# Kernel tuning notes

Measured on AMD Instinct MI355X. Metric: run time of the kernel, lower is better.

## Reference

```python
import jax, jax.numpy as jnp
import numpy as np

B, N, D = 4, 2048, 1024
DF = 4 * D
EPS = 1e-5


def _layernorm(x, w, b):
    mu = jnp.mean(x, axis=-1, keepdims=True)
    var = jnp.mean(jnp.square(x - mu), axis=-1, keepdims=True)
    return (x - mu) * jax.lax.rsqrt(var + EPS) * w + b


def setup_inputs() -> dict:
    key = jax.random.key(0)
    ks = jax.random.split(key, 8)
    x = jax.random.normal(ks[0], (B, N, D), dtype=jnp.float32)
    # conv filter param (torch init is zeros; use small randn for numeric coverage)
    weights = jax.random.normal(ks[1], (1, 1, N), dtype=jnp.float32) * 0.02
    # registered buffer: sqrt(1/(i+1)) per token, shape (1, N, 1)
    scale = jnp.sqrt(1.0 / (jnp.arange(N, dtype=jnp.float32) + 1.0))[None, :, None]
    ln1_w = jnp.ones((D,), jnp.float32)
    ln1_b = jnp.zeros((D,), jnp.float32)
    W1 = jax.random.normal(ks[2], (DF, D), dtype=jnp.float32) * 0.02
    b1 = jnp.zeros((DF,), jnp.float32)
    W2 = jax.random.normal(ks[3], (D, DF), dtype=jnp.float32) * 0.02
    b2 = jnp.zeros((D,), jnp.float32)
    scalar = jax.random.normal(ks[4], (1,), dtype=jnp.float32) * 0.1
    ln2_w = jnp.ones((D,), jnp.float32)
    ln2_b = jnp.zeros((D,), jnp.float32)
    return dict(x=x, weights=weights, scale=scale, ln1_w=ln1_w, ln1_b=ln1_b,
                W1=W1, b1=b1, W2=W2, b2=b2, scalar=scalar, ln2_w=ln2_w, ln2_b=ln2_b)


def reference(x, weights, scale, ln1_w, ln1_b, W1, b1, W2, b2, scalar, ln2_w, ln2_b):
    n = weights.shape[-1]
    # FFT token-mixing conv: operate over token axis. x: (B,N,D) -> (B,D,N)
    xt = jnp.swapaxes(x, -2, -1)
    # real inputs -> rfft/irfft equals real(ifft(fft*fft)) from the torch code
    prod = jnp.fft.rfft(xt, n=2 * n) * jnp.fft.rfft(weights, n=2 * n)
    conv = jnp.fft.irfft(prod, n=2 * n)[..., :n]  # (B,D,N)
    x1 = jnp.swapaxes(conv, -2, -1)               # (B,N,D)
    x1 = _layernorm(x + x1 * scale, ln1_w, ln1_b)
    # GELU MLP (torch F.gelu default = exact erf gelu)
    h = jax.nn.gelu(jnp.einsum('bnd,fd->bnf', x1, W1) + b1, approximate=False)
    mlp = jnp.einsum('bnf,df->bnd', h, W2) + b2
    x2 = _layernorm(x1 + scalar * mlp, ln2_w, ln2_b)
    return x2
```

## Files before the change

### kernel.cpp

```cpp
#include <hip/hip_runtime.h>
#include <cstdint>

typedef float floatx4 __attribute__((ext_vector_type(4)));
typedef int intx8 __attribute__((ext_vector_type(8)));

__device__ __forceinline__ unsigned short f2b(float f) {
  union { float f; unsigned u; } v; v.f = f;
  return (unsigned short)((v.u + 0x7FFFu + ((v.u >> 16) & 1u)) >> 16);
}
__device__ __forceinline__ float b2f(unsigned short h) {
  union { unsigned u; float f; } v; v.u = ((unsigned)h) << 16;
  return v.f;
}

__device__ __forceinline__ void gload_lds16(const void* g, void* l) {
  __builtin_amdgcn_global_load_lds(
      (const __attribute__((address_space(1))) void*)g,
      (__attribute__((address_space(3))) void*)l, 16, 0, 0);
}


__global__ void cast_f8x64_kernel(const float* __restrict__ in,
                                  int* __restrict__ out) {
  long i = (long)blockIdx.x * 256 + threadIdx.x;
  float4 v = ((const float4*)in)[i];
  int pk = __builtin_amdgcn_cvt_pk_fp8_f32(v.x * 64.0f, v.y * 64.0f, 0, false);
  pk = __builtin_amdgcn_cvt_pk_fp8_f32(v.z * 64.0f, v.w * 64.0f, pk, true);
  out[i] = pk;
}

__global__ void build_T8_kernel(const float* __restrict__ w,
                                int* __restrict__ T8) {
  long i = (long)blockIdx.x * 256 + threadIdx.x;
  int n = (int)(i >> 9);
  int m0 = (int)(i & 511) * 4;
  float v[4];
#pragma unroll
  for (int r = 0; r < 4; ++r) {
    int m = m0 + r;
    v[r] = (m <= n) ? w[n - m] * 64.0f : 0.0f;
  }
  int pk = __builtin_amdgcn_cvt_pk_fp8_f32(v[0], v[1], 0, false);
  pk = __builtin_amdgcn_cvt_pk_fp8_f32(v[2], v[3], pk, true);
  T8[i] = pk;
}

__global__ void transpose_cast_f8_kernel(const float* __restrict__ x,
                                         unsigned char* __restrict__ xT) {
  __shared__ float tile[32][33];
  int b = blockIdx.z;
  int n0 = blockIdx.y * 32;
  int d0 = blockIdx.x * 32;
  int tx = threadIdx.x;
  int ty = threadIdx.y;
  for (int i = ty; i < 32; i += 8)
    tile[i][tx] = x[((long)b * 2048 + n0 + i) * 1024 + d0 + tx];
  __syncthreads();
  float a = tile[ty * 4 + 0][tx];
  float c = tile[ty * 4 + 1][tx];
  float e = tile[ty * 4 + 2][tx];
  float f = tile[ty * 4 + 3][tx];
  int pk = __builtin_amdgcn_cvt_pk_fp8_f32(a, c, 0, false);
  pk = __builtin_amdgcn_cvt_pk_fp8_f32(e, f, pk, true);
  *(int*)(xT + ((long)b * 1024 + d0 + tx) * 2048 + n0 + ty * 4) = pk;
}

template <int EPI, int NT, bool TRI>
__global__ __launch_bounds__(256, 2) void gemm_f8(
    const unsigned char* __restrict__ A, const unsigned char* __restrict__ B,
    int Kstride, int Kloop, long zsA, long zsB, long zsC,
    int rx, int ryb, int gxn, unsigned sclA, unsigned sclB,
    const float* __restrict__ resid, const float* __restrict__ scale,
    const float* __restrict__ bias,
    float* __restrict__ Cf, unsigned short* __restrict__ Cb,
    unsigned char* __restrict__ C8) {
  __shared__ __align__(16) unsigned char As[2 * 16 * 1040];
  __shared__ __align__(16) unsigned char Bs[2 * 16 * 1040];
  const int tid = threadIdx.x;
  const int wid = tid >> 6;
  const int lane = tid & 63;
  const int quad = lane >> 4;
  const int l16 = lane & 15;
  const int wm = (wid >> 1) * 64;
  const int wn = (wid & 1) * 64;

  const int bid = blockIdx.x;
  const int xcd = bid & 7;
  const int ib = bid >> 3;
  const int ci = ib % rx;
  const int ri = ib / rx;
  long bm, bn;
  if (TRI) {
    bm = (long)(ri == 0 ? xcd : 15 - xcd) * 128;
    bn = (long)ci * 128;
  } else {
    const int gx = xcd % gxn;
    const int gy = xcd / gxn;
    bm = (long)(gy * ryb + ri) * 128;
    bn = (long)(gx * rx + ci) * 128;
  }
  const int bz = blockIdx.z;
  const unsigned char* Ab = A + zsA * bz;
  const unsigned char* Bb = B + zsB * bz;

  floatx4 acc[4][4];
#pragma unroll
  for (int i = 0; i < 4; ++i)
#pragma unroll
    for (int j = 0; j < 4; ++j)
      acc[i][j] = floatx4{0.0f, 0.0f, 0.0f, 0.0f};

  const int srow = tid >> 3;
  const int scol = (tid & 7) * 16;
  const unsigned char* gA[4];
  const unsigned char* gB[4];
  unsigned char* lA[4];
  unsigned char* lB[4];
#pragma unroll
  for (int p = 0; p < 4; ++p) {
    gA[p] = Ab + (bm + p * 32 + srow) * (long)Kstride + scol;
    gB[p] = Bb + (bn + p * 32 + srow) * (long)Kstride + scol;
    lA[p] = As + (p * 4 + wid) * 1040;
    lB[p] = Bs + (p * 4 + wid) * 1040;
  }

  int offA[4], offB[4];
#pragma unroll
  for (int i = 0; i < 4; ++i) {
    const int ra = wm + i * 16 + l16;
    offA[i] = (ra >> 3) * 1040 + (ra & 7) * 128 + quad * 32;
    const int rb = wn + i * 16 + l16;
    offB[i] = (rb >> 3) * 1040 + (rb & 7) * 128 + quad * 32;
  }

  const int kend = TRI ? min(Kloop, (int)bm + 128) : Kloop;

#pragma unroll
  for (int p = 0; p < 4; ++p) {
    gload_lds16(gA[p], lA[p]);
    gload_lds16(gB[p], lB[p]);
  }

  int so = 0;
  for (int kk = 0; kk < kend; kk += 128) {
    const int kn = kk + 128;
    if (kn < kend) {
      const int po = so ^ 16640;
#pragma unroll
      for (int p = 0; p < 4; ++p) {
        gload_lds16(gA[p] + kn, lA[p] + po);
        gload_lds16(gB[p] + kn, lB[p] + po);
      }
      asm volatile("s_waitcnt vmcnt(8)" ::: "memory");
    } else {
      asm volatile("s_waitcnt vmcnt(0)" ::: "memory");
    }
    __builtin_amdgcn_s_barrier();

    intx8 af[4], bfr[4];
#pragma unroll
    for (int i = 0; i < 4; ++i) {
      union { intx8 v; int4 q[2]; } u;
      u.q[0] = *(const int4*)(As + so + offA[i]);
      u.q[1] = *(const int4*)(As + so + offA[i] + 16);
      af[i] = u.v;
    }
#pragma unroll
    for (int j = 0; j < 4; ++j) {
      union { intx8 v; int4 q[2]; } u;
      u.q[0] = *(const int4*)(Bs + so + offB[j]);
      u.q[1] = *(const int4*)(Bs + so + offB[j] + 16);
      bfr[j] = u.v;
    }
    __builtin_amdgcn_s_setprio(1);
#pragma unroll
    for (int i = 0; i < 4; ++i)
#pragma unroll
      for (int j = 0; j < 4; ++j)
        acc[i][j] = __builtin_amdgcn_mfma_scale_f32_16x16x128_f8f6f4(
            af[i], bfr[j], acc[i][j], 0 , 0 ,
            0, sclA, 0, sclB);
    __builtin_amdgcn_s_setprio(0);
    __builtin_amdgcn_s_barrier();
    so ^= 16640;
  }

#pragma unroll
  for (int i = 0; i < 4; ++i)
#pragma unroll
    for (int j = 0; j < 4; ++j)
#pragma unroll
      for (int r = 0; r < 4; ++r) {
        long row = bm + wm + i * 16 + quad * 4 + r;
        long col = bn + wn + j * 16 + l16;
        long idx = (long)bz * zsC + row * (long)NT + col;
        float v = acc[i][j][r];
        if (EPI == 0) {
          Cb[idx] = f2b(v);
        } else if (EPI == 1) {
          Cf[idx] = resid[idx] + scale[row] * v;
        } else {
          v += bias[col];
          float u = v * (0.7978845608f + 0.0356774081f * v * v);
          float u2 = u * u;
          float t = __fdividef(u * (15.0f + u2), 15.0f + 6.0f * u2);
          t = fminf(fmaxf(t, -1.0f), 1.0f);
          float g = 0.5f * v * (1.0f + t);
          int pk = __builtin_amdgcn_cvt_pk_fp8_f32(g, 0.0f, 0, false);
          C8[idx] = (unsigned char)(pk & 0xFF);
        }
      }
}

__global__ __launch_bounds__(256) void ln_kernel(
    const float* __restrict__ in, const float* __restrict__ w,
    const float* __restrict__ b, unsigned short* __restrict__ outb,
    int* __restrict__ outf8) {
  const long row = blockIdx.x;
  const int tid = threadIdx.x;
  float4 v = ((const float4*)in)[row * 256 + tid];
  float s = v.x + v.y + v.z + v.w;
  float ss = v.x * v.x + v.y * v.y + v.z * v.z + v.w * v.w;
#pragma unroll
  for (int off = 32; off > 0; off >>= 1) {
    s += __shfl_down(s, off);
    ss += __shfl_down(ss, off);
  }
  __shared__ float red[8];
  const int wid = tid >> 6, lane = tid & 63;
  if (lane == 0) { red[wid] = s; red[4 + wid] = ss; }
  __syncthreads();
  s = red[0] + red[1] + red[2] + red[3];
  ss = red[4] + red[5] + red[6] + red[7];
  const float mu = s * (1.0f / 1024.0f);
  const float var = ss * (1.0f / 1024.0f) - mu * mu;
  const float rs = rsqrtf(var + 1e-5f);
  float4 wv = ((const float4*)w)[tid];
  float4 bv = ((const float4*)b)[tid];
  float o0 = (v.x - mu) * rs * wv.x + bv.x;
  float o1 = (v.y - mu) * rs * wv.y + bv.y;
  float o2 = (v.z - mu) * rs * wv.z + bv.z;
  float o3 = (v.w - mu) * rs * wv.w + bv.w;
  ushort4 u{f2b(o0), f2b(o1), f2b(o2), f2b(o3)};
  ((ushort4*)outb)[row * 256 + tid] = u;
  int pk = __builtin_amdgcn_cvt_pk_fp8_f32(o0, o1, 0, false);
  pk = __builtin_amdgcn_cvt_pk_fp8_f32(o2, o3, pk, true);
  outf8[row * 256 + tid] = pk;
}

__global__ __launch_bounds__(256) void ln2_fused_kernel(
    const unsigned short* __restrict__ y0, const unsigned short* __restrict__ y1,
    const unsigned short* __restrict__ x1b, const float* __restrict__ b2,
    const float* __restrict__ scalar_p, const float* __restrict__ w,
    const float* __restrict__ b, float* __restrict__ out) {
  const long row = blockIdx.x;
  const int tid = threadIdx.x;
  ushort4 a4 = ((const ushort4*)y0)[row * 256 + tid];
  ushort4 c4 = ((const ushort4*)y1)[row * 256 + tid];
  ushort4 xr = ((const ushort4*)x1b)[row * 256 + tid];
  float4 bias = ((const float4*)b2)[tid];
  const float scl = scalar_p[0];
  float4 v;
  v.x = b2f(xr.x) + scl * (b2f(a4.x) + b2f(c4.x) + bias.x);
  v.y = b2f(xr.y) + scl * (b2f(a4.y) + b2f(c4.y) + bias.y);
  v.z = b2f(xr.z) + scl * (b2f(a4.z) + b2f(c4.z) + bias.z);
  v.w = b2f(xr.w) + scl * (b2f(a4.w) + b2f(c4.w) + bias.w);
  float s = v.x + v.y + v.z + v.w;
  float ss = v.x * v.x + v.y * v.y + v.z * v.z + v.w * v.w;
#pragma unroll
  for (int off = 32; off > 0; off >>= 1) {
    s += __shfl_down(s, off);
    ss += __shfl_down(ss, off);
  }
  __shared__ float red[8];
  const int wid = tid >> 6, lane = tid & 63;
  if (lane == 0) { red[wid] = s; red[4 + wid] = ss; }
  __syncthreads();
  s = red[0] + red[1] + red[2] + red[3];
  ss = red[4] + red[5] + red[6] + red[7];
  const float mu = s * (1.0f / 1024.0f);
  const float var = ss * (1.0f / 1024.0f) - mu * mu;
  const float rs = rsqrtf(var + 1e-5f);
  float4 wv = ((const float4*)w)[tid];
  float4 bv = ((const float4*)b)[tid];
  float4 o;
  o.x = (v.x - mu) * rs * wv.x + bv.x;
  o.y = (v.y - mu) * rs * wv.y + bv.y;
  o.z = (v.z - mu) * rs * wv.z + bv.z;
  o.w = (v.w - mu) * rs * wv.w + bv.w;
  ((float4*)out)[row * 256 + tid] = o;
}

extern "C" void kernel_launch(void* const* d_in, const int* in_sizes, int n_in,
                              void* d_out, int out_size, void* d_ws, size_t ws_size,
                              hipStream_t stream) {
  const float* x      = (const float*)d_in[0];
  const float* wconv  = (const float*)d_in[1];
  const float* scale  = (const float*)d_in[2];
  const float* ln1w   = (const float*)d_in[3];
  const float* ln1b   = (const float*)d_in[4];
  const float* W1     = (const float*)d_in[5];
  const float* b1     = (const float*)d_in[6];
  const float* W2     = (const float*)d_in[7];
  const float* b2     = (const float*)d_in[8];
  const float* scalar = (const float*)d_in[9];
  const float* ln2w   = (const float*)d_in[10];
  const float* ln2b   = (const float*)d_in[11];
  float* out = (float*)d_out;

  const unsigned SCL_1  = 0x7F7F7F7Fu;
  const unsigned SCL_64 = 0x79797979u;

  char* ws = (char*)d_ws;
  unsigned char* xT8   = (unsigned char*)ws;  ws += (size_t)4 * 1024 * 2048;
  unsigned char* T8    = (unsigned char*)ws;  ws += (size_t)2048 * 2048;
  unsigned char* W1f8  = (unsigned char*)ws;  ws += (size_t)4096 * 1024;
  unsigned char* W2f8  = (unsigned char*)ws;  ws += (size_t)4096 * 1024;
  float* y             = (float*)ws;          ws += (size_t)8192 * 1024 * 4;
  unsigned short* yb   = (unsigned short*)ws; ws += (size_t)2 * 8192 * 1024 * 2;
  unsigned short* x1b  = (unsigned short*)ws; ws += (size_t)8192 * 1024 * 2;
  unsigned char* x1f8  = (unsigned char*)ws;  ws += (size_t)8192 * 1024;
  unsigned char* h8    = (unsigned char*)ws;  ws += (size_t)8192 * 4096;

  cast_f8x64_kernel<<<4096, 256, 0, stream>>>(W1, (int*)W1f8);
  cast_f8x64_kernel<<<4096, 256, 0, stream>>>(W2, (int*)W2f8);
  build_T8_kernel<<<4096, 256, 0, stream>>>(wconv, (int*)T8);
  transpose_cast_f8_kernel<<<dim3(32, 64, 4), dim3(32, 8), 0, stream>>>(x, xT8);

  gemm_f8<1, 1024, true><<<dim3(128, 1, 4), 256, 0, stream>>>(
      T8, xT8, 2048, 2048, 0L, (long)1024 * 2048, (long)2048 * 1024,
      8, 0, 0, SCL_64, SCL_1, x, scale, nullptr, y, nullptr, nullptr);
  ln_kernel<<<8192, 256, 0, stream>>>(y, ln1w, ln1b, x1b, (int*)x1f8);
  gemm_f8<2, 4096, false><<<dim3(2048, 1, 1), 256, 0, stream>>>(
      x1f8, W1f8, 1024, 1024, 0L, 0L, 0L,
      16, 16, 2, SCL_1, SCL_64, nullptr, nullptr, b1, nullptr, nullptr, h8);
  gemm_f8<0, 1024, false><<<dim3(512, 1, 2), 256, 0, stream>>>(
      h8, W2f8, 4096, 2048, 2048L, 2048L, (long)8192 * 1024,
      8, 8, 1, SCL_1, SCL_64, nullptr, nullptr, nullptr, nullptr, yb, nullptr);
  ln2_fused_kernel<<<8192, 256, 0, stream>>>(
      yb, yb + (size_t)8192 * 1024, x1b, b2, scalar, ln2w, ln2b, out);
}
```

Baseline: 297.9 us.

## Use 256x256-tile 512-thread FP8 GEMM for MLP; single-buffer conv GEMM

Adds a new gemm_f8_256 kernel with 256x256 output tiles, 8 waves and double-buffered LDS, and uses it for both MLP GEMMs. Larger tiles raise data reuse per LDS load and cut global traffic. The original 128x128 kernel, still used for the triangular conv GEMM, drops its double buffering and priority hints so it can run at 4 blocks per CU, trading load/compute overlap for occupancy. Fewer, larger blocks may hurt wave balance across CUs, and the extra accumulators raise register pressure.

After: 301.1 us. Within noise of the previous version (+1.1%).

```diff
diff --git a/kernel.cpp b/kernel.cpp
--- a/kernel.cpp
+++ b/kernel.cpp
@@ -66,7 +66,7 @@
 }
 
 template <int EPI, int NT, bool TRI>
-__global__ __launch_bounds__(256, 2) void gemm_f8(
+__global__ __launch_bounds__(256, 4) void gemm_f8(
     const unsigned char* __restrict__ A, const unsigned char* __restrict__ B,
     int Kstride, int Kloop, long zsA, long zsB, long zsC,
     int rx, int ryb, int gxn, unsigned sclA, unsigned sclB,
@@ -74,8 +74,8 @@
     const float* __restrict__ bias,
     float* __restrict__ Cf, unsigned short* __restrict__ Cb,
     unsigned char* __restrict__ C8) {
-  __shared__ __align__(16) unsigned char As[2 * 16 * 1040];
-  __shared__ __align__(16) unsigned char Bs[2 * 16 * 1040];
+  __shared__ __align__(16) unsigned char As[16 * 1040];
+  __shared__ __align__(16) unsigned char Bs[16 * 1040];
   const int tid = threadIdx.x;
   const int wid = tid >> 6;
   const int lane = tid & 63;
@@ -124,55 +124,34 @@
     lB[p] = Bs + (p * 4 + wid) * 1040;
   }
 
-  int offA[4], offB[4];
-#pragma unroll
-  for (int i = 0; i < 4; ++i) {
-    const int ra = wm + i * 16 + l16;
-    offA[i] = (ra >> 3) * 1040 + (ra & 7) * 128 + quad * 32;
-    const int rb = wn + i * 16 + l16;
-    offB[i] = (rb >> 3) * 1040 + (rb & 7) * 128 + quad * 32;
-  }
-
   const int kend = TRI ? min(Kloop, (int)bm + 128) : Kloop;
-
-#pragma unroll
-  for (int p = 0; p < 4; ++p) {
-    gload_lds16(gA[p], lA[p]);
-    gload_lds16(gB[p], lB[p]);
-  }
-
-  int so = 0;
   for (int kk = 0; kk < kend; kk += 128) {
-    const int kn = kk + 128;
-    if (kn < kend) {
-      const int po = so ^ 16640;
-#pragma unroll
-      for (int p = 0; p < 4; ++p) {
-        gload_lds16(gA[p] + kn, lA[p] + po);
-        gload_lds16(gB[p] + kn, lB[p] + po);
-      }
-      asm volatile("s_waitcnt vmcnt(8)" ::: "memory");
-    } else {
-      asm volatile("s_waitcnt vmcnt(0)" ::: "memory");
-    }
-    __builtin_amdgcn_s_barrier();
-
+    __syncthreads();
+#pragma unroll
+    for (int p = 0; p < 4; ++p) {
+      gload_lds16(gA[p] + kk, lA[p]);
+      gload_lds16(gB[p] + kk, lB[p]);
+    }
+    __syncthreads();
     intx8 af[4], bfr[4];
 #pragma unroll
     for (int i = 0; i < 4; ++i) {
+      const int ra = wm + i * 16 + l16;
+      const int off = (ra >> 3) * 1040 + (ra & 7) * 128 + quad * 32;
       union { intx8 v; int4 q[2]; } u;
-      u.q[0] = *(const int4*)(As + so + offA[i]);
-      u.q[1] = *(const int4*)(As + so + offA[i] + 16);
+      u.q[0] = *(const int4*)(As + off);
+      u.q[1] = *(const int4*)(As + off + 16);
       af[i] = u.v;
     }
 #pragma unroll
     for (int j = 0; j < 4; ++j) {
+      const int rb = wn + j * 16 + l16;
+      const int off = (rb >> 3) * 1040 + (rb & 7) * 128 + quad * 32;
       union { intx8 v; int4 q[2]; } u;
-      u.q[0] = *(const int4*)(Bs + so + offB[j]);
-      u.q[1] = *(const int4*)(Bs + so + offB[j] + 16);
+      u.q[0] = *(const int4*)(Bs + off);
+      u.q[1] = *(const int4*)(Bs + off + 16);
       bfr[j] = u.v;
     }
-    __builtin_amdgcn_s_setprio(1);
 #pragma unroll
     for (int i = 0; i < 4; ++i)
 #pragma unroll
@@ -180,9 +159,6 @@
         acc[i][j] = __builtin_amdgcn_mfma_scale_f32_16x16x128_f8f6f4(
             af[i], bfr[j], acc[i][j], 0 , 0 ,
             0, sclA, 0, sclB);
-    __builtin_amdgcn_s_setprio(0);
-    __builtin_amdgcn_s_barrier();
-    so ^= 16640;
   }
 
 #pragma unroll
@@ -212,6 +188,142 @@
       }
 }
 
+template <int EPI, int NT>
+__global__ __launch_bounds__(512, 2) void gemm_f8_256(
+    const unsigned char* __restrict__ A, const unsigned char* __restrict__ B,
+    int Kstride, int Kloop, long zsA, long zsB, long zsC,
+    int rx, int ryb, int gxn, unsigned sclA, unsigned sclB,
+    const float* __restrict__ bias,
+    unsigned short* __restrict__ Cb, unsigned char* __restrict__ C8) {
+  __shared__ __align__(16) unsigned char As[2 * 32 * 1040];
+  __shared__ __align__(16) unsigned char Bs[2 * 32 * 1040];
+  const int tid = threadIdx.x;
+  const int wid = tid >> 6;
+  const int lane = tid & 63;
+  const int quad = lane >> 4;
+  const int l16 = lane & 15;
+  const int wm = (wid >> 2) * 128;
+  const int wn = (wid & 3) * 64;
+
+  const int bid = blockIdx.x;
+  const int xcd = bid & 7;
+  const int ib = bid >> 3;
+  const int ci = ib % rx;
+  const int ri = ib / rx;
+  const int gx = xcd % gxn;
+  const int gy = xcd / gxn;
+  const long bm = (long)(gy * ryb + ri) * 256;
+  const long bn = (long)(gx * rx + ci) * 256;
+  const int bz = blockIdx.z;
+  const unsigned char* Ab = A + zsA * bz;
+  const unsigned char* Bb = B + zsB * bz;
+
+  floatx4 acc[8][4];
+#pragma unroll
+  for (int i = 0; i < 8; ++i)
+#pragma unroll
+    for (int j = 0; j < 4; ++j)
+      acc[i][j] = floatx4{0.0f, 0.0f, 0.0f, 0.0f};
+
+  const int srow = wid * 8 + (lane >> 3);
+  const int scol = (lane & 7) * 16;
+  const unsigned char* gA[4];
+  const unsigned char* gB[4];
+  unsigned char* lA[4];
+  unsigned char* lB[4];
+#pragma unroll
+  for (int p = 0; p < 4; ++p) {
+    gA[p] = Ab + (bm + p * 64 + srow) * (long)Kstride + scol;
+    gB[p] = Bb + (bn + p * 64 + srow) * (long)Kstride + scol;
+    lA[p] = As + (p * 8 + wid) * 1040;
+    lB[p] = Bs + (p * 8 + wid) * 1040;
+  }
+
+  int offA[8], offB[4];
+#pragma unroll
+  for (int i = 0; i < 8; ++i) {
+    const int ra = wm + i * 16 + l16;
+    offA[i] = (ra >> 3) * 1040 + (ra & 7) * 128 + quad * 32;
+  }
+#pragma unroll
+  for (int j = 0; j < 4; ++j) {
+    const int rb = wn + j * 16 + l16;
+    offB[j] = (rb >> 3) * 1040 + (rb & 7) * 128 + quad * 32;
+  }
+
+#pragma unroll
+  for (int p = 0; p < 4; ++p) {
+    gload_lds16(gA[p], lA[p]);
+    gload_lds16(gB[p], lB[p]);
+  }
+
+  int so = 0;
+  for (int kk = 0; kk < Kloop; kk += 128) {
+    const int kn = kk + 128;
+    if (kn < Kloop) {
+      const int po = so ^ 33280;
+#pragma unroll
+      for (int p = 0; p < 4; ++p) {
+        gload_lds16(gA[p] + kn, lA[p] + po);
+        gload_lds16(gB[p] + kn, lB[p] + po);
+      }
+      asm volatile("s_waitcnt vmcnt(8)" ::: "memory");
+    } else {
+      asm volatile("s_waitcnt vmcnt(0)" ::: "memory");
+    }
+    __builtin_amdgcn_s_barrier();
+
+    intx8 bfr[4];
+#pragma unroll
+    for (int j = 0; j < 4; ++j) {
+      union { intx8 v; int4 q[2]; } u;
+      u.q[0] = *(const int4*)(Bs + so + offB[j]);
+      u.q[1] = *(const int4*)(Bs + so + offB[j] + 16);
+      bfr[j] = u.v;
+    }
+    __builtin_amdgcn_s_setprio(1);
+#pragma unroll
+    for (int i = 0; i < 8; ++i) {
+      union { intx8 v; int4 q[2]; } u;
+      u.q[0] = *(const int4*)(As + so + offA[i]);
+      u.q[1] = *(const int4*)(As + so + offA[i] + 16);
+      intx8 af = u.v;
+#pragma unroll
+      for (int j = 0; j < 4; ++j)
+        acc[i][j] = __builtin_amdgcn_mfma_scale_f32_16x16x128_f8f6f4(
+            af, bfr[j], acc[i][j], 0 , 0 ,
+            0, sclA, 0, sclB);
+    }
+    __builtin_amdgcn_s_setprio(0);
+    __builtin_amdgcn_s_barrier();
+    so ^= 33280;
+  }
+
+#pragma unroll
+  for (int i = 0; i < 8; ++i)
+#pragma unroll
+    for (int j = 0; j < 4; ++j)
+#pragma unroll
+      for (int r = 0; r < 4; ++r) {
+        long row = bm + wm + i * 16 + quad * 4 + r;
+        long col = bn + wn + j * 16 + l16;
+        long idx = (long)bz * zsC + row * (long)NT + col;
+        float v = acc[i][j][r];
+        if (EPI == 0) {
+          Cb[idx] = f2b(v);
+        } else {
+          v += bias[col];
+          float u = v * (0.7978845608f + 0.0356774081f * v * v);
+          float u2 = u * u;
+          float t = __fdividef(u * (15.0f + u2), 15.0f + 6.0f * u2);
+          t = fminf(fmaxf(t, -1.0f), 1.0f);
+          float g = 0.5f * v * (1.0f + t);
+          int pk = __builtin_amdgcn_cvt_pk_fp8_f32(g, 0.0f, 0, false);
+          C8[idx] = (unsigned char)(pk & 0xFF);
+        }
+      }
+}
+
 __global__ __launch_bounds__(256) void ln_kernel(
     const float* __restrict__ in, const float* __restrict__ w,
     const float* __restrict__ b, unsigned short* __restrict__ outb,
@@ -331,12 +443,12 @@
       T8, xT8, 2048, 2048, 0L, (long)1024 * 2048, (long)2048 * 1024,
       8, 0, 0, SCL_64, SCL_1, x, scale, nullptr, y, nullptr, nullptr);
   ln_kernel<<<8192, 256, 0, stream>>>(y, ln1w, ln1b, x1b, (int*)x1f8);
-  gemm_f8<2, 4096, false><<<dim3(2048, 1, 1), 256, 0, stream>>>(
+  gemm_f8_256<2, 4096><<<dim3(512, 1, 1), 512, 0, stream>>>(
       x1f8, W1f8, 1024, 1024, 0L, 0L, 0L,
-      16, 16, 2, SCL_1, SCL_64, nullptr, nullptr, b1, nullptr, nullptr, h8);
-  gemm_f8<0, 1024, false><<<dim3(512, 1, 2), 256, 0, stream>>>(
+      8, 8, 2, SCL_1, SCL_64, b1, nullptr, h8);
+  gemm_f8_256<0, 1024><<<dim3(128, 1, 2), 512, 0, stream>>>(
       h8, W2f8, 4096, 2048, 2048L, 2048L, (long)8192 * 1024,
-      8, 8, 1, SCL_1, SCL_64, nullptr, nullptr, nullptr, nullptr, yb, nullptr);
+      4, 4, 1, SCL_1, SCL_64, nullptr, yb, nullptr);
   ln2_fused_kernel<<<8192, 256, 0, stream>>>(
       yb, yb + (size_t)8192 * 1024, x1b, b2, scalar, ln2w, ln2b, out);
 }
```
